# Optimization experiments

Measured on AMD Instinct MI355X. Metric: run time of the kernel, lower is better.

## Reference

```python
import jax, jax.numpy as jnp
import numpy as np

N = 200000
E = 3200000
F_IN = 128
D = 64
G = 512
T = 10


def setup_inputs() -> dict:
    key = jax.random.key(0)
    ks = jax.random.split(key, 20)
    def lin(k, out_d, in_d):
        kw, kb = jax.random.split(k)
        s = 1.0 / np.sqrt(in_d)
        W = jax.random.uniform(kw, (out_d, in_d), jnp.float32, -s, s)
        b = jax.random.uniform(kb, (out_d,), jnp.float32, -s, s)
        return W, b
    x = jax.random.normal(ks[0], (N, F_IN), jnp.float32)
    edge_index = jax.random.randint(ks[1], (2, E), 0, N, jnp.int32)
    batch = jnp.sort(jax.random.randint(ks[2], (N,), 0, G, jnp.int32))
    Wc0, bc0 = lin(ks[3], D, F_IN)
    Wc1, bc1 = lin(ks[4], D, D)
    Wc2, bc2 = lin(ks[5], D, D)
    Wc3, bc3 = lin(ks[6], D, D)
    Wmax, bmax = lin(ks[7], D, D)
    W1, b1 = lin(ks[8], D, 4 * D)
    W2, b2 = lin(ks[9], T, D)
    return {"x": x, "edge_index": edge_index, "batch": batch, "num_graphs": G,
            "Wc0": Wc0, "bc0": bc0, "Wc1": Wc1, "bc1": bc1,
            "Wc2": Wc2, "bc2": bc2, "Wc3": Wc3, "bc3": bc3,
            "Wmax": Wmax, "bmax": bmax, "W1": W1, "b1": b1, "W2": W2, "b2": b2}


def gcn_conv(x, W, b, src, dst, n):
    # PyG GCNConv: h = x W^T; add self-loops; sym-normalize by (deg+1)^-1/2
    h = x @ W.T  # [n, D]
    deg = jax.ops.segment_sum(jnp.ones_like(dst, jnp.float32), dst, num_segments=n) + 1.0
    dis = deg ** -0.5  # deg >= 1 always (self loop)
    coef = (dis[src] * dis[dst])[:, None]  # [E,1]
    agg = jax.ops.segment_sum(h[src] * coef, dst, num_segments=n)
    agg = agg + h * (dis * dis)[:, None]  # self-loop contribution
    return agg + b


def reference(x, edge_index, batch, num_graphs,
              Wc0, bc0, Wc1, bc1, Wc2, bc2, Wc3, bc3,
              Wmax, bmax, W1, b1, W2, b2):
    n = x.shape[0]
    src, dst = edge_index[0], edge_index[1]
    convs = [(Wc0, bc0), (Wc1, bc1), (Wc2, bc2), (Wc3, bc3)]
    h = x
    h_all = []
    for (W, b) in convs:
        h = gcn_conv(h, W, b, src, dst, n)
        h = jax.nn.relu(h @ Wmax.T + bmax)
        h_all.append(h)
    hcat = jnp.concatenate(h_all, axis=1)  # [n, 4*D]
    pooled = jax.ops.segment_max(hcat, batch, num_segments=num_graphs)
    pooled = jnp.where(jnp.isfinite(pooled), pooled, 0.0)  # empty graphs -> 0
    out = jax.nn.relu(pooled @ W1.T + b1)
    return out @ W2.T + b2
```

## Files before the change

kernel.cpp:

```cpp
#include <hip/hip_runtime.h>
#include <hip/hip_bf16.h>
#include <math.h>

constexpr int N_NODES = 200000;
constexpr int E_EDGES = 3200000;
constexpr int F_IN    = 128;
constexpr int D       = 64;
constexpr int G_GRAPHS = 512;
constexpr int T_OUT   = 10;

constexpr int SCAN_CHUNK   = 2048;
constexpr int SCAN_NBLOCKS = (N_NODES + SCAN_CHUNK - 1) / SCAN_CHUNK;

__global__ __launch_bounds__(256) void deg_kernel(const int* __restrict__ dst,
                                                  int* __restrict__ deg) {
    int e = blockIdx.x * 256 + threadIdx.x;
    if (e < E_EDGES) atomicAdd(&deg[dst[e]], 1);
}

__global__ __launch_bounds__(256) void dis_kernel(const int* __restrict__ deg,
                                                  float* __restrict__ dis) {
    int i = blockIdx.x * 256 + threadIdx.x;
    if (i < N_NODES) dis[i] = 1.0f / sqrtf((float)deg[i] + 1.0f);
}

__global__ __launch_bounds__(256) void scan_p1(const int* __restrict__ deg,
                                               int* __restrict__ bsum) {
    const int b = blockIdx.x, t = threadIdx.x;
    int idx0 = b * SCAN_CHUNK + t * 8;
    int s = 0;
    #pragma unroll
    for (int i = 0; i < 8; ++i) {
        int idx = idx0 + i;
        if (idx < N_NODES) s += deg[idx];
    }
    #pragma unroll
    for (int off = 32; off; off >>= 1) s += __shfl_down(s, off, 64);
    __shared__ int ws[4];
    if ((t & 63) == 0) ws[t >> 6] = s;
    __syncthreads();
    if (t == 0) bsum[b] = ws[0] + ws[1] + ws[2] + ws[3];
}

__global__ __launch_bounds__(128) void scan_p2(int* __restrict__ bsum,
                                               int* __restrict__ row_ptr) {
    __shared__ int tmp[128];
    const int t = threadIdx.x;
    int v = (t < SCAN_NBLOCKS) ? bsum[t] : 0;
    tmp[t] = v;
    __syncthreads();
    #pragma unroll
    for (int off = 1; off < 128; off <<= 1) {
        int u = (t >= off) ? tmp[t - off] : 0;
        __syncthreads();
        tmp[t] += u;
        __syncthreads();
    }
    if (t < SCAN_NBLOCKS) bsum[t] = tmp[t] - v;
    if (t == 0) row_ptr[N_NODES] = E_EDGES;
}

__global__ __launch_bounds__(256) void scan_p3(const int* __restrict__ deg,
                                               const int* __restrict__ bsum,
                                               int* __restrict__ row_ptr) {
    const int b = blockIdx.x, t = threadIdx.x;
    int idx0 = b * SCAN_CHUNK + t * 8;
    int loc[8];
    int s = 0;
    #pragma unroll
    for (int i = 0; i < 8; ++i) {
        int idx = idx0 + i;
        loc[i] = (idx < N_NODES) ? deg[idx] : 0;
        s += loc[i];
    }
    __shared__ int tmp[256];
    tmp[t] = s;
    __syncthreads();
    #pragma unroll
    for (int off = 1; off < 256; off <<= 1) {
        int u = (t >= off) ? tmp[t - off] : 0;
        __syncthreads();
        tmp[t] += u;
        __syncthreads();
    }
    int run = tmp[t] - s + bsum[b];
    #pragma unroll
    for (int i = 0; i < 8; ++i) {
        int idx = idx0 + i;
        if (idx < N_NODES) row_ptr[idx] = run;
        run += loc[i];
    }
}

__global__ __launch_bounds__(256) void place_kernel(const int* __restrict__ src,
                                                    const int* __restrict__ dst,
                                                    const float* __restrict__ dis,
                                                    const int* __restrict__ row_ptr,
                                                    int* __restrict__ cursor,
                                                    int* __restrict__ csr_src,
                                                    float* __restrict__ csr_coef) {
    int e = blockIdx.x * 256 + threadIdx.x;
    if (e < E_EDGES) {
        int s = src[e], d = dst[e];
        int pos = row_ptr[d] + atomicAdd(&cursor[d], 1);
        csr_src[pos]  = s;
        csr_coef[pos] = dis[s] * dis[d];
    }
}

template<int K, bool FUSED_MAX>
__global__ __launch_bounds__(256) void gemm_k(const float* __restrict__ in,
                                              const float* __restrict__ W,
                                              float* __restrict__ out,
                                              const float* __restrict__ bias,
                                              const int* __restrict__ batch,
                                              int* __restrict__ pooled,
                                              int layer) {
    constexpr int GPR = K / 4;
    __shared__ float smem[64 * K + D * K];
    __shared__ int   bs[64];
    float* Xs = smem;
    float* Ws = smem + 64 * K;
    const int tid = threadIdx.x;
    const size_t row0 = (size_t)blockIdx.x * 64;

    for (int li = tid; li < 64 * GPR; li += 256) {
        int r = li / GPR, g = li % GPR;
        float4 v = *(const float4*)(in + (row0 + r) * K + g * 4);
        int gs = g ^ ((r >> 2) & 7);
        *(float4*)(Xs + r * K + gs * 4) = v;
    }
    for (int li = tid; li < D * GPR; li += 256) {
        int r = li / GPR, g = li % GPR;
        float4 v = *(const float4*)(W + r * K + g * 4);
        int gs = g ^ ((r >> 2) & 7);
        *(float4*)(Ws + r * K + gs * 4) = v;
    }
    if (FUSED_MAX && tid < 64) bs[tid] = batch[row0 + tid];
    __syncthreads();

    const int lane = tid & 63;
    const int wave = tid >> 6;
    const int rg = lane & 15;
    const int cg = wave * 4 + (lane >> 4);
    float acc[4][4] = {};
    #pragma unroll 8
    for (int kq = 0; kq < GPR; ++kq) {
        float4 xv[4], wv[4];
        #pragma unroll
        for (int i = 0; i < 4; ++i)
            xv[i] = *(const float4*)(Xs + (rg * 4 + i) * K + ((kq ^ (rg & 7)) * 4));
        #pragma unroll
        for (int j = 0; j < 4; ++j)
            wv[j] = *(const float4*)(Ws + (cg * 4 + j) * K + ((kq ^ (cg & 7)) * 4));
        #pragma unroll
        for (int i = 0; i < 4; ++i)
            #pragma unroll
            for (int j = 0; j < 4; ++j)
                acc[i][j] += xv[i].x * wv[j].x + xv[i].y * wv[j].y +
                             xv[i].z * wv[j].z + xv[i].w * wv[j].w;
    }

    if constexpr (FUSED_MAX) {
        __syncthreads();
        float* Ts = smem;
        #pragma unroll
        for (int i = 0; i < 4; ++i) {
            size_t r = row0 + rg * 4 + i;
            float4 o;
            float* op = (float*)&o;
            #pragma unroll
            for (int j = 0; j < 4; ++j)
                op[j] = fmaxf(acc[i][j] + bias[cg * 4 + j], 0.0f);
            *(float4*)(out + r * D + cg * 4) = o;
            *(float4*)(Ts + (rg * 4 + i) * 68 + cg * 4) = o;
        }
        __syncthreads();
        if (tid < 64) {
            const int col = tid;
            float m = Ts[col];
            int bg = bs[0];
            #pragma unroll 8
            for (int r = 1; r < 64; ++r) {
                int b2 = bs[r];
                float v = Ts[r * 68 + col];
                if (b2 != bg) {
                    atomicMax(&pooled[bg * (4 * D) + layer * D + col], __float_as_int(m));
                    bg = b2; m = v;
                } else {
                    m = fmaxf(m, v);
                }
            }
            atomicMax(&pooled[bg * (4 * D) + layer * D + col], __float_as_int(m));
        }
    } else {
        #pragma unroll
        for (int i = 0; i < 4; ++i) {
            size_t r = row0 + rg * 4 + i;
            float4 o = make_float4(acc[i][0], acc[i][1], acc[i][2], acc[i][3]);
            *(float4*)(out + r * D + cg * 4) = o;
        }
    }
}

__global__ __launch_bounds__(256) void agg_kernel(const int* __restrict__ row_ptr,
                                                  const int* __restrict__ csr_src,
                                                  const float* __restrict__ csr_coef,
                                                  const float* __restrict__ Lbuf,
                                                  const float* __restrict__ dis,
                                                  const float* __restrict__ bias,
                                                  float* __restrict__ A) {
    int v = __builtin_amdgcn_readfirstlane((int)(blockIdx.x * 4) + (int)(threadIdx.x >> 6));
    if (v >= N_NODES) return;
    const int lane = threadIdx.x & 63;
    const int beg = row_ptr[v];
    const int end = row_ptr[v + 1];
    float dd = dis[v];
    float acc = Lbuf[(size_t)v * D + lane] * (dd * dd) + bias[lane];
    #pragma unroll 4
    for (int p = beg; p < end; ++p) {
        int s = csr_src[p];
        float c = csr_coef[p];
        acc += Lbuf[(size_t)s * D + lane] * c;
    }
    A[(size_t)v * D + lane] = acc;
}

__global__ __launch_bounds__(64) void mlp_kernel(const float* __restrict__ pooled,
                                                 const float* __restrict__ W1,
                                                 const float* __restrict__ b1,
                                                 const float* __restrict__ W2,
                                                 const float* __restrict__ b2,
                                                 float* __restrict__ out) {
    __shared__ float ps[4 * D];
    __shared__ float hs[D];
    const int g = blockIdx.x, t = threadIdx.x;
    *(float4*)(ps + t * 4) = *(const float4*)(pooled + (size_t)g * (4 * D) + t * 4);
    __syncthreads();
    float acc = b1[t];
    const float* w = W1 + (size_t)t * (4 * D);
    #pragma unroll 4
    for (int k = 0; k < 4 * D; k += 4) {
        float4 wv = *(const float4*)(w + k);
        float4 pv = *(const float4*)(ps + k);
        acc += wv.x * pv.x + wv.y * pv.y + wv.z * pv.z + wv.w * pv.w;
    }
    hs[t] = fmaxf(acc, 0.0f);
    __syncthreads();
    if (t < T_OUT) {
        float o = b2[t];
        const float* w2 = W2 + t * D;
        #pragma unroll
        for (int k = 0; k < D; ++k) o += hs[k] * w2[k];
        out[(size_t)g * T_OUT + t] = o;
    }
}

extern "C" void kernel_launch(void* const* d_in, const int* in_sizes, int n_in,
                              void* d_out, int out_size, void* d_ws, size_t ws_size,
                              hipStream_t stream) {
    (void)in_sizes; (void)n_in; (void)out_size; (void)ws_size;
    const float* x     = (const float*)d_in[0];
    const int*   ei    = (const int*)d_in[1];
    const int*   batch = (const int*)d_in[2];
    const float* Wc[4] = {(const float*)d_in[4], (const float*)d_in[6],
                          (const float*)d_in[8], (const float*)d_in[10]};
    const float* bc[4] = {(const float*)d_in[5], (const float*)d_in[7],
                          (const float*)d_in[9], (const float*)d_in[11]};
    const float* Wmax = (const float*)d_in[12];
    const float* bmax = (const float*)d_in[13];
    const float* W1   = (const float*)d_in[14];
    const float* b1   = (const float*)d_in[15];
    const float* W2   = (const float*)d_in[16];
    const float* b2   = (const float*)d_in[17];
    float* out = (float*)d_out;

    float* fws = (float*)d_ws;
    size_t off = 0;
    float* L        = fws + off; off += (size_t)N_NODES * D;
    float* A        = fws + off; off += (size_t)N_NODES * D;
    int*   csr_src  = (int*)(fws + off); off += E_EDGES;
    float* csr_coef = fws + off; off += E_EDGES;
    int*   row_ptr  = (int*)(fws + off); off += N_NODES + 16;
    int*   deg      = (int*)(fws + off); off += N_NODES;
    int*   cursor   = (int*)(fws + off); off += N_NODES;
    float* dis      = fws + off; off += N_NODES;
    int*   pooled   = (int*)(fws + off); off += G_GRAPHS * 4 * D;
    int*   bsum     = (int*)(fws + off); off += SCAN_NBLOCKS + 16;

    const int* srcI = ei;
    const int* dstI = ei + E_EDGES;

    hipMemsetAsync(deg,    0, sizeof(int) * N_NODES, stream);
    hipMemsetAsync(cursor, 0, sizeof(int) * N_NODES, stream);
    hipMemsetAsync(pooled, 0, sizeof(int) * G_GRAPHS * 4 * D, stream);

    deg_kernel <<<(E_EDGES + 255) / 256, 256, 0, stream>>>(dstI, deg);
    dis_kernel <<<(N_NODES + 255) / 256, 256, 0, stream>>>(deg, dis);
    scan_p1<<<SCAN_NBLOCKS, 256, 0, stream>>>(deg, bsum);
    scan_p2<<<1, 128, 0, stream>>>(bsum, row_ptr);
    scan_p3<<<SCAN_NBLOCKS, 256, 0, stream>>>(deg, bsum, row_ptr);
    place_kernel<<<(E_EDGES + 255) / 256, 256, 0, stream>>>(srcI, dstI, dis, row_ptr,
                                                            cursor, csr_src, csr_coef);

    const float* cur = x;
    for (int l = 0; l < 4; ++l) {
        if (l == 0)
            gemm_k<F_IN, false><<<N_NODES / 64, 256, 0, stream>>>(cur, Wc[0], L,
                                                                  nullptr, nullptr, nullptr, 0);
        else
            gemm_k<D, false><<<N_NODES / 64, 256, 0, stream>>>(cur, Wc[l], L,
                                                               nullptr, nullptr, nullptr, 0);
        agg_kernel<<<N_NODES / 4, 256, 0, stream>>>(row_ptr, csr_src, csr_coef,
                                                    L, dis, bc[l], A);
        gemm_k<D, true><<<N_NODES / 64, 256, 0, stream>>>(A, Wmax, L,
                                                          bmax, batch, pooled, l);
        cur = L;
    }
    mlp_kernel<<<G_GRAPHS, 64, 0, stream>>>((const float*)pooled, W1, b1, W2, b2, out);
}
```

Baseline: 1.456 ms.

## Fold GCN normalization into GEMM row scaling and bucket CSR placement by destination range

The symmetric normalization dis[s]*dis[d] is factored out: the feature GEMM now scales each output row by dis[src], and the aggregation sums unscaled neighbor rows before multiplying by dis[dst] and adding bias. This removes the per-edge coefficient array, so aggregation reads only neighbor indices and the 12.8 MB coefficient buffer is neither written nor read. CSR placement is split into four passes over destination-node ranges, which narrows the scatter and atomic footprint of each pass. In exchange, the edge list is read four times and three extra kernels are launched.

```diff
diff --git a/kernel.cpp b/kernel.cpp
--- a/kernel.cpp
+++ b/kernel.cpp
@@ -11,6 +11,9 @@
 
 constexpr int SCAN_CHUNK   = 2048;
 constexpr int SCAN_NBLOCKS = (N_NODES + SCAN_CHUNK - 1) / SCAN_CHUNK;
+
+constexpr int PLACE_NPASS = 4;
+constexpr int PLACE_RANGE = N_NODES / PLACE_NPASS;
 
 __global__ __launch_bounds__(256) void deg_kernel(const int* __restrict__ dst,
                                                   int* __restrict__ deg) {
@@ -92,33 +95,39 @@
     }
 }
 
-__global__ __launch_bounds__(256) void place_kernel(const int* __restrict__ src,
-                                                    const int* __restrict__ dst,
-                                                    const float* __restrict__ dis,
-                                                    const int* __restrict__ row_ptr,
-                                                    int* __restrict__ cursor,
-                                                    int* __restrict__ csr_src,
-                                                    float* __restrict__ csr_coef) {
-    int e = blockIdx.x * 256 + threadIdx.x;
-    if (e < E_EDGES) {
-        int s = src[e], d = dst[e];
-        int pos = row_ptr[d] + atomicAdd(&cursor[d], 1);
-        csr_src[pos]  = s;
-        csr_coef[pos] = dis[s] * dis[d];
-    }
-}
-
-template<int K, bool FUSED_MAX>
+__global__ __launch_bounds__(256) void place_pass(const int* __restrict__ src,
+                                                  const int* __restrict__ dst,
+                                                  const int* __restrict__ row_ptr,
+                                                  int* __restrict__ cursor,
+                                                  int* __restrict__ csr_src,
+                                                  int lo, int hi) {
+    int e0 = (blockIdx.x * 256 + threadIdx.x) * 4;
+    if (e0 >= E_EDGES) return;
+    int4 d4 = *(const int4*)(dst + e0);
+    const int* dp = (const int*)&d4;
+    #pragma unroll
+    for (int i = 0; i < 4; ++i) {
+        int d = dp[i];
+        if (d >= lo && d < hi) {
+            int pos = row_ptr[d] + atomicAdd(&cursor[d], 1);
+            csr_src[pos] = src[e0 + i];
+        }
+    }
+}
+
+template<int K, bool FUSED_MAX, bool SCALE>
 __global__ __launch_bounds__(256) void gemm_k(const float* __restrict__ in,
                                               const float* __restrict__ W,
                                               float* __restrict__ out,
                                               const float* __restrict__ bias,
                                               const int* __restrict__ batch,
                                               int* __restrict__ pooled,
+                                              const float* __restrict__ dis,
                                               int layer) {
     constexpr int GPR = K / 4;
     __shared__ float smem[64 * K + D * K];
     __shared__ int   bs[64];
+    __shared__ float ds[64];
     float* Xs = smem;
     float* Ws = smem + 64 * K;
     const int tid = threadIdx.x;
@@ -137,6 +146,7 @@
         *(float4*)(Ws + r * K + gs * 4) = v;
     }
     if (FUSED_MAX && tid < 64) bs[tid] = batch[row0 + tid];
+    if (SCALE && tid < 64)     ds[tid] = dis[row0 + tid];
     __syncthreads();
 
     const int lane = tid & 63;
@@ -197,7 +207,9 @@
         #pragma unroll
         for (int i = 0; i < 4; ++i) {
             size_t r = row0 + rg * 4 + i;
-            float4 o = make_float4(acc[i][0], acc[i][1], acc[i][2], acc[i][3]);
+            float sc = SCALE ? ds[rg * 4 + i] : 1.0f;
+            float4 o = make_float4(acc[i][0] * sc, acc[i][1] * sc,
+                                   acc[i][2] * sc, acc[i][3] * sc);
             *(float4*)(out + r * D + cg * 4) = o;
         }
     }
@@ -205,7 +217,6 @@
 
 __global__ __launch_bounds__(256) void agg_kernel(const int* __restrict__ row_ptr,
                                                   const int* __restrict__ csr_src,
-                                                  const float* __restrict__ csr_coef,
                                                   const float* __restrict__ Lbuf,
                                                   const float* __restrict__ dis,
                                                   const float* __restrict__ bias,
@@ -215,15 +226,13 @@
     const int lane = threadIdx.x & 63;
     const int beg = row_ptr[v];
     const int end = row_ptr[v + 1];
-    float dd = dis[v];
-    float acc = Lbuf[(size_t)v * D + lane] * (dd * dd) + bias[lane];
+    float acc = Lbuf[(size_t)v * D + lane];
     #pragma unroll 4
     for (int p = beg; p < end; ++p) {
         int s = csr_src[p];
-        float c = csr_coef[p];
-        acc += Lbuf[(size_t)s * D + lane] * c;
-    }
-    A[(size_t)v * D + lane] = acc;
+        acc += Lbuf[(size_t)s * D + lane];
+    }
+    A[(size_t)v * D + lane] = acc * dis[v] + bias[lane];
 }
 
 __global__ __launch_bounds__(64) void mlp_kernel(const float* __restrict__ pooled,
@@ -280,7 +289,6 @@
     float* L        = fws + off; off += (size_t)N_NODES * D;
     float* A        = fws + off; off += (size_t)N_NODES * D;
     int*   csr_src  = (int*)(fws + off); off += E_EDGES;
-    float* csr_coef = fws + off; off += E_EDGES;
     int*   row_ptr  = (int*)(fws + off); off += N_NODES + 16;
     int*   deg      = (int*)(fws + off); off += N_NODES;
     int*   cursor   = (int*)(fws + off); off += N_NODES;
@@ -300,21 +308,24 @@
     scan_p1<<<SCAN_NBLOCKS, 256, 0, stream>>>(deg, bsum);
     scan_p2<<<1, 128, 0, stream>>>(bsum, row_ptr);
     scan_p3<<<SCAN_NBLOCKS, 256, 0, stream>>>(deg, bsum, row_ptr);
-    place_kernel<<<(E_EDGES + 255) / 256, 256, 0, stream>>>(srcI, dstI, dis, row_ptr,
-                                                            cursor, csr_src, csr_coef);
+    for (int p = 0; p < PLACE_NPASS; ++p)
+        place_pass<<<E_EDGES / (256 * 4), 256, 0, stream>>>(srcI, dstI, row_ptr,
+                                                            cursor, csr_src,
+                                                            p * PLACE_RANGE,
+                                                            (p + 1) * PLACE_RANGE);
 
     const float* cur = x;
     for (int l = 0; l < 4; ++l) {
         if (l == 0)
-            gemm_k<F_IN, false><<<N_NODES / 64, 256, 0, stream>>>(cur, Wc[0], L,
-                                                                  nullptr, nullptr, nullptr, 0);
+            gemm_k<F_IN, false, true><<<N_NODES / 64, 256, 0, stream>>>(
+                cur, Wc[0], L, nullptr, nullptr, nullptr, dis, 0);
         else
-            gemm_k<D, false><<<N_NODES / 64, 256, 0, stream>>>(cur, Wc[l], L,
-                                                               nullptr, nullptr, nullptr, 0);
-        agg_kernel<<<N_NODES / 4, 256, 0, stream>>>(row_ptr, csr_src, csr_coef,
+            gemm_k<D, false, true><<<N_NODES / 64, 256, 0, stream>>>(
+                cur, Wc[l], L, nullptr, nullptr, nullptr, dis, 0);
+        agg_kernel<<<N_NODES / 4, 256, 0, stream>>>(row_ptr, csr_src,
                                                     L, dis, bc[l], A);
-        gemm_k<D, true><<<N_NODES / 64, 256, 0, stream>>>(A, Wmax, L,
-                                                          bmax, batch, pooled, l);
+        gemm_k<D, true, false><<<N_NODES / 64, 256, 0, stream>>>(
+            A, Wmax, L, bmax, batch, pooled, nullptr, l);
         cur = L;
     }
     mlp_kernel<<<G_GRAPHS, 64, 0, stream>>>((const float*)pooled, W1, b1, W2, b2, out);
```

New measurement: 1.365 ms. 1.07x faster.
